# Optimization experiments

Measured on AMD Instinct MI355X. Metric: run time of the kernel, lower is better.

## Reference

```python
import jax, jax.numpy as jnp
import numpy as np

R_MAX = 32
S_MAX = 2
TOKEN_Z = 128
B, N = 1, 1024
NUM_POS = 2 * R_MAX + 2      # 66 bins for residue-index distance
NUM_TOK = 2 * R_MAX + 2      # 66 bins for token-index distance
NUM_CHAIN = 2 * S_MAX + 2    # 6 bins for chain (symmetry) distance
D_IN = NUM_POS + NUM_TOK + 1 + NUM_CHAIN  # 139 = 4*(r_max+1) + 2*(s_max+1) + 1


def setup_inputs() -> dict:
    key = jax.random.key(0)
    ks = jax.random.split(key, 6)
    asym_id = jax.random.randint(ks[0], (B, N), 0, 4)
    residue_index = jax.random.randint(ks[1], (B, N), 0, 512)
    entity_id = jax.random.randint(ks[2], (B, N), 0, 2)
    token_index = jax.random.randint(ks[3], (B, N), 0, 1024)
    sym_id = jax.random.randint(ks[4], (B, N), 0, 4)
    W = jax.random.normal(ks[5], (D_IN, TOKEN_Z), dtype=jnp.float32) / np.sqrt(D_IN).astype(np.float32)
    return {
        'asym_id': asym_id,
        'residue_index': residue_index,
        'entity_id': entity_id,
        'token_index': token_index,
        'sym_id': sym_id,
        'W': W,
    }


def _bin_indices(asym_id, residue_index, token_index, sym_id):
    """Compute the per-pair bin index for each of the three one-hot features."""
    same_chain = asym_id[:, :, None] == asym_id[:, None, :]            # [B,N,N]
    same_residue = residue_index[:, :, None] == residue_index[:, None, :]

    d_res = jnp.clip(residue_index[:, :, None] - residue_index[:, None, :] + R_MAX, 0, 2 * R_MAX)
    d_res = jnp.where(same_chain, d_res, 2 * R_MAX + 1)

    d_tok = jnp.clip(token_index[:, :, None] - token_index[:, None, :] + R_MAX, 0, 2 * R_MAX)
    d_tok = jnp.where(same_chain & same_residue, d_tok, 2 * R_MAX + 1)

    d_chain = jnp.clip(sym_id[:, :, None] - sym_id[:, None, :] + S_MAX, 0, 2 * S_MAX)
    d_chain = jnp.where(same_chain, 2 * S_MAX + 1, d_chain)
    return d_res, d_tok, d_chain


def reference(asym_id, residue_index, entity_id, token_index, sym_id, W):
    # Fused gather-sum: one_hot(d) @ W_block == W_block[d], so the concat of
    # one-hots followed by LinearNoBias equals a sum of 3 row-gathers from W
    # plus the same-entity flag times one W row. Identical math to the
    # original, without materializing the [B,N,N,139] one-hot/concat tensor.
    d_res, d_tok, d_chain = _bin_indices(asym_id, residue_index, token_index, sym_id)
    same_entity = (entity_id[:, :, None] == entity_id[:, None, :]).astype(W.dtype)  # [B,N,N]

    W_pos = W[:NUM_POS]                                  # [66, Z]
    W_tok = W[NUM_POS:NUM_POS + NUM_TOK]                 # [66, Z]
    w_ent = W[NUM_POS + NUM_TOK]                         # [Z]
    W_chain = W[NUM_POS + NUM_TOK + 1:]                  # [6, Z]

    p = W_pos[d_res] + W_tok[d_tok] + W_chain[d_chain] + same_entity[..., None] * w_ent
    return p  # [B, N, N, token_z]
```

## Files before the change

kernel.cpp:

```cpp
#include <hip/hip_runtime.h>


#define N_TOK   1024
#define R_MAX   32
#define S_MAX   2
#define ROW_POS   0
#define ROW_TOK   66
#define ROW_ENT   132
#define ROW_CHAIN 133

__global__ __launch_bounds__(256) void relpos_kernel(
    const int*   __restrict__ asym_id,
    const int*   __restrict__ residue_index,
    const int*   __restrict__ entity_id,
    const int*   __restrict__ token_index,
    const int*   __restrict__ sym_id,
    const float* __restrict__ W,
    float*       __restrict__ out)
{
    __shared__ int s_idx[64];

    const int tid = threadIdx.x;
    const int i   = blockIdx.x >> 4;
    const int j0  = (blockIdx.x & 15) << 6;

    if (tid < 64) {
        const int j  = j0 + tid;
        const int ai = asym_id[i],       aj = asym_id[j];
        const int ri = residue_index[i], rj = residue_index[j];
        const int ti = token_index[i],   tj = token_index[j];
        const int si = sym_id[i],        sj = sym_id[j];
        const int ei = entity_id[i],     ej = entity_id[j];

        const bool same_chain = (ai == aj);
        const bool same_res   = (ri == rj);

        int d_res = min(max(ri - rj + R_MAX, 0), 2 * R_MAX);
        if (!same_chain) d_res = 2 * R_MAX + 1;

        int d_tok = min(max(ti - tj + R_MAX, 0), 2 * R_MAX);
        if (!(same_chain && same_res)) d_tok = 2 * R_MAX + 1;

        const int d_chain = same_chain ? (2 * S_MAX + 1)
                                       : min(max(si - sj + S_MAX, 0), 2 * S_MAX);
        const int ent = (ei == ej) ? 1 : 0;

        s_idx[tid] = d_res | (d_tok << 7) | (d_chain << 14) | (ent << 17);
    }
    __syncthreads();

    const int slot    = tid & 31;
    const int plocal0 = tid >> 5;

    const float4* __restrict__ W4 = (const float4*)W;
    const float4 e = W4[ROW_ENT * 32 + slot];

    float4* __restrict__ outp = (float4*)out + ((long long)blockIdx.x << 11);

    #pragma unroll
    for (int iter = 0; iter < 8; ++iter) {
        const int pl      = plocal0 + iter * 8;
        const int packed  = s_idx[pl];
        const int d_res   =  packed        & 127;
        const int d_tok   = (packed >> 7)  & 127;
        const int d_chain = (packed >> 14) & 7;
        const float m     = (packed & (1 << 17)) ? 1.0f : 0.0f;

        const float4 a = W4[(ROW_POS   + d_res)   * 32 + slot];
        const float4 b = W4[(ROW_TOK   + d_tok)   * 32 + slot];
        const float4 c = W4[(ROW_CHAIN + d_chain) * 32 + slot];

        float4 r;
        r.x = a.x + b.x + c.x + m * e.x;
        r.y = a.y + b.y + c.y + m * e.y;
        r.z = a.z + b.z + c.z + m * e.z;
        r.w = a.w + b.w + c.w + m * e.w;

        outp[pl * 32 + slot] = r;
    }
}

extern "C" void kernel_launch(void* const* d_in, const int* in_sizes, int n_in,
                              void* d_out, int out_size, void* d_ws, size_t ws_size,
                              hipStream_t stream) {
    const int*   asym_id       = (const int*)d_in[0];
    const int*   residue_index = (const int*)d_in[1];
    const int*   entity_id     = (const int*)d_in[2];
    const int*   token_index   = (const int*)d_in[3];
    const int*   sym_id        = (const int*)d_in[4];
    const float* W             = (const float*)d_in[5];
    float*       out           = (float*)d_out;

    const int grid  = (N_TOK * N_TOK) / 64;
    const int block = 256;

    relpos_kernel<<<grid, block, 0, stream>>>(
        asym_id, residue_index, entity_id, token_index, sym_id, W, out);
}
```

Before: 106.4 us.

## Precompute combined row table so each pair output is a single gather

Adds a small pre-kernel that precomputes all 270 reachable sums of position, token, chain and entity rows into a workspace table. The main kernel then computes one combined index per pair and copies one table row, replacing three gathers plus adds. This cuts L2/L1 gather traffic and ALU work per output element, at the cost of an extra kernel launch. It needs enough workspace and falls back to the original direct kernel otherwise.

```diff
diff --git a/kernel.cpp b/kernel.cpp
--- a/kernel.cpp
+++ b/kernel.cpp
@@ -8,17 +8,57 @@
 #define ROW_TOK   66
 #define ROW_ENT   132
 #define ROW_CHAIN 133
+#define TBL_BASE  135
+#define TBL_ROWS  270
+#define TBL_BYTES (TBL_ROWS * 128 * 4)
 
-__global__ __launch_bounds__(256) void relpos_kernel(
+__global__ __launch_bounds__(256) void build_table(
+    const float* __restrict__ W, float* __restrict__ tbl)
+{
+    const int t = blockIdx.x * blockDim.x + threadIdx.x;
+    if (t >= TBL_ROWS * 32) return;
+    const int id   = t >> 5;
+    const int slot = t & 31;
+    const int ent  = (id >= TBL_BASE) ? 1 : 0;
+    const int base = id - ent * TBL_BASE;
+
+    const float4* __restrict__ W4 = (const float4*)W;
+    float4 p, k, c;
+    if (base < 5) {
+        p = W4[(ROW_POS   + 65)   * 32 + slot];
+        k = W4[(ROW_TOK   + 65)   * 32 + slot];
+        c = W4[(ROW_CHAIN + base) * 32 + slot];
+    } else if (base < 70) {
+        p = W4[(ROW_POS + (base - 5)) * 32 + slot];
+        k = W4[(ROW_TOK   + 65)   * 32 + slot];
+        c = W4[(ROW_CHAIN + 5)    * 32 + slot];
+    } else {
+        p = W4[(ROW_POS   + 32)   * 32 + slot];
+        k = W4[(ROW_TOK + (base - 70)) * 32 + slot];
+        c = W4[(ROW_CHAIN + 5)    * 32 + slot];
+    }
+    float4 r;
+    r.x = p.x + k.x + c.x;
+    r.y = p.y + k.y + c.y;
+    r.z = p.z + k.z + c.z;
+    r.w = p.w + k.w + c.w;
+    if (ent) {
+        const float4 e = W4[ROW_ENT * 32 + slot];
+        r.x += e.x; r.y += e.y; r.z += e.z; r.w += e.w;
+    }
+    ((float4*)tbl)[id * 32 + slot] = r;
+}
+
+__global__ __launch_bounds__(256) void relpos_tbl(
     const int*   __restrict__ asym_id,
     const int*   __restrict__ residue_index,
     const int*   __restrict__ entity_id,
     const int*   __restrict__ token_index,
     const int*   __restrict__ sym_id,
-    const float* __restrict__ W,
+    const float* __restrict__ tbl,
     float*       __restrict__ out)
 {
-    __shared__ int s_idx[64];
+    __shared__ int s_id[64];
 
     const int tid = threadIdx.x;
     const int i   = blockIdx.x >> 4;
@@ -32,29 +72,70 @@
         const int si = sym_id[i],        sj = sym_id[j];
         const int ei = entity_id[i],     ej = entity_id[j];
 
+        int base;
+        if (ai != aj) {
+            base = min(max(si - sj + S_MAX, 0), 2 * S_MAX);
+        } else if (ri != rj) {
+            base = 5 + min(max(ri - rj + R_MAX, 0), 2 * R_MAX);
+        } else {
+            base = 70 + min(max(ti - tj + R_MAX, 0), 2 * R_MAX);
+        }
+        s_id[tid] = base + ((ei == ej) ? TBL_BASE : 0);
+    }
+    __syncthreads();
+
+    const int slot    = tid & 31;
+    const int plocal0 = tid >> 5;
+
+    const float4* __restrict__ T4 = (const float4*)tbl;
+    float4* __restrict__ outp = (float4*)out + ((long long)blockIdx.x << 11);
+
+    #pragma unroll
+    for (int iter = 0; iter < 8; ++iter) {
+        const int pl = plocal0 + iter * 8;
+        const int id = s_id[pl];
+        outp[pl * 32 + slot] = T4[id * 32 + slot];
+    }
+}
+
+__global__ __launch_bounds__(256) void relpos_direct(
+    const int*   __restrict__ asym_id,
+    const int*   __restrict__ residue_index,
+    const int*   __restrict__ entity_id,
+    const int*   __restrict__ token_index,
+    const int*   __restrict__ sym_id,
+    const float* __restrict__ W,
+    float*       __restrict__ out)
+{
+    __shared__ int s_idx[64];
+    const int tid = threadIdx.x;
+    const int i   = blockIdx.x >> 4;
+    const int j0  = (blockIdx.x & 15) << 6;
+
+    if (tid < 64) {
+        const int j  = j0 + tid;
+        const int ai = asym_id[i],       aj = asym_id[j];
+        const int ri = residue_index[i], rj = residue_index[j];
+        const int ti = token_index[i],   tj = token_index[j];
+        const int si = sym_id[i],        sj = sym_id[j];
+        const int ei = entity_id[i],     ej = entity_id[j];
         const bool same_chain = (ai == aj);
         const bool same_res   = (ri == rj);
-
         int d_res = min(max(ri - rj + R_MAX, 0), 2 * R_MAX);
         if (!same_chain) d_res = 2 * R_MAX + 1;
-
         int d_tok = min(max(ti - tj + R_MAX, 0), 2 * R_MAX);
         if (!(same_chain && same_res)) d_tok = 2 * R_MAX + 1;
-
         const int d_chain = same_chain ? (2 * S_MAX + 1)
                                        : min(max(si - sj + S_MAX, 0), 2 * S_MAX);
         const int ent = (ei == ej) ? 1 : 0;
-
         s_idx[tid] = d_res | (d_tok << 7) | (d_chain << 14) | (ent << 17);
     }
     __syncthreads();
 
     const int slot    = tid & 31;
     const int plocal0 = tid >> 5;
-
     const float4* __restrict__ W4 = (const float4*)W;
     const float4 e = W4[ROW_ENT * 32 + slot];
-
     float4* __restrict__ outp = (float4*)out + ((long long)blockIdx.x << 11);
 
     #pragma unroll
@@ -65,17 +146,14 @@
         const int d_tok   = (packed >> 7)  & 127;
         const int d_chain = (packed >> 14) & 7;
         const float m     = (packed & (1 << 17)) ? 1.0f : 0.0f;
-
         const float4 a = W4[(ROW_POS   + d_res)   * 32 + slot];
         const float4 b = W4[(ROW_TOK   + d_tok)   * 32 + slot];
         const float4 c = W4[(ROW_CHAIN + d_chain) * 32 + slot];
-
         float4 r;
         r.x = a.x + b.x + c.x + m * e.x;
         r.y = a.y + b.y + c.y + m * e.y;
         r.z = a.z + b.z + c.z + m * e.z;
         r.w = a.w + b.w + c.w + m * e.w;
-
         outp[pl * 32 + slot] = r;
     }
 }
@@ -94,6 +172,13 @@
     const int grid  = (N_TOK * N_TOK) / 64;
     const int block = 256;
 
-    relpos_kernel<<<grid, block, 0, stream>>>(
-        asym_id, residue_index, entity_id, token_index, sym_id, W, out);
+    if (ws_size >= (size_t)TBL_BYTES) {
+        float* tbl = (float*)d_ws;
+        build_table<<<(TBL_ROWS * 32 + 255) / 256, 256, 0, stream>>>(W, tbl);
+        relpos_tbl<<<grid, block, 0, stream>>>(
+            asym_id, residue_index, entity_id, token_index, sym_id, tbl, out);
+    } else {
+        relpos_direct<<<grid, block, 0, stream>>>(
+            asym_id, residue_index, entity_id, token_index, sym_id, W, out);
+    }
 }
```

Result: slower. 110.1 us (+3.5%).

## Process eight tiles per block with double-buffered index computation

Applied to the files above, without the earlier changes.

Each block now handles eight 64-pair tiles instead of one, so the grid shrinks eightfold. While the current tile is gathered and written, the first wave precomputes the packed bin indices for the next tile into a second shared buffer. The aim is to cut block launch overhead and hide the index-load latency. The cost is a __syncthreads per tile and fewer blocks to spread across the GPU.

```diff
diff --git a/kernel.cpp b/kernel.cpp
--- a/kernel.cpp
+++ b/kernel.cpp
@@ -9,6 +9,36 @@
 #define ROW_ENT   132
 #define ROW_CHAIN 133
 
+#define TILES_PER_BLOCK 8
+#define NUM_BLOCKS ((N_TOK * N_TOK / 64) / TILES_PER_BLOCK)
+
+__device__ __forceinline__ int pack_idx(
+    const int* __restrict__ asym_id, const int* __restrict__ residue_index,
+    const int* __restrict__ entity_id, const int* __restrict__ token_index,
+    const int* __restrict__ sym_id, int i, int j)
+{
+    const int ai = asym_id[i],       aj = asym_id[j];
+    const int ri = residue_index[i], rj = residue_index[j];
+    const int ti = token_index[i],   tj = token_index[j];
+    const int si = sym_id[i],        sj = sym_id[j];
+    const int ei = entity_id[i],     ej = entity_id[j];
+
+    const bool same_chain = (ai == aj);
+    const bool same_res   = (ri == rj);
+
+    int d_res = min(max(ri - rj + R_MAX, 0), 2 * R_MAX);
+    if (!same_chain) d_res = 2 * R_MAX + 1;
+
+    int d_tok = min(max(ti - tj + R_MAX, 0), 2 * R_MAX);
+    if (!(same_chain && same_res)) d_tok = 2 * R_MAX + 1;
+
+    const int d_chain = same_chain ? (2 * S_MAX + 1)
+                                   : min(max(si - sj + S_MAX, 0), 2 * S_MAX);
+    const int ent = (ei == ej) ? 1 : 0;
+
+    return d_res | (d_tok << 7) | (d_chain << 14) | (ent << 17);
+}
+
 __global__ __launch_bounds__(256) void relpos_kernel(
     const int*   __restrict__ asym_id,
     const int*   __restrict__ residue_index,
@@ -18,34 +48,17 @@
     const float* __restrict__ W,
     float*       __restrict__ out)
 {
-    __shared__ int s_idx[64];
+    __shared__ int s_id[2][64];
 
-    const int tid = threadIdx.x;
-    const int i   = blockIdx.x >> 4;
-    const int j0  = (blockIdx.x & 15) << 6;
+    const int tid   = threadIdx.x;
+    const int tile0 = blockIdx.x * TILES_PER_BLOCK;
 
     if (tid < 64) {
-        const int j  = j0 + tid;
-        const int ai = asym_id[i],       aj = asym_id[j];
-        const int ri = residue_index[i], rj = residue_index[j];
-        const int ti = token_index[i],   tj = token_index[j];
-        const int si = sym_id[i],        sj = sym_id[j];
-        const int ei = entity_id[i],     ej = entity_id[j];
-
-        const bool same_chain = (ai == aj);
-        const bool same_res   = (ri == rj);
-
-        int d_res = min(max(ri - rj + R_MAX, 0), 2 * R_MAX);
-        if (!same_chain) d_res = 2 * R_MAX + 1;
-
-        int d_tok = min(max(ti - tj + R_MAX, 0), 2 * R_MAX);
-        if (!(same_chain && same_res)) d_tok = 2 * R_MAX + 1;
-
-        const int d_chain = same_chain ? (2 * S_MAX + 1)
-                                       : min(max(si - sj + S_MAX, 0), 2 * S_MAX);
-        const int ent = (ei == ej) ? 1 : 0;
-
-        s_idx[tid] = d_res | (d_tok << 7) | (d_chain << 14) | (ent << 17);
+        const int tile = tile0;
+        const int i  = tile >> 4;
+        const int j  = ((tile & 15) << 6) + tid;
+        s_id[0][tid] = pack_idx(asym_id, residue_index, entity_id,
+                                token_index, sym_id, i, j);
     }
     __syncthreads();
 
@@ -55,28 +68,43 @@
     const float4* __restrict__ W4 = (const float4*)W;
     const float4 e = W4[ROW_ENT * 32 + slot];
 
-    float4* __restrict__ outp = (float4*)out + ((long long)blockIdx.x << 11);
+    for (int t = 0; t < TILES_PER_BLOCK; ++t) {
+        const int buf = t & 1;
 
-    #pragma unroll
-    for (int iter = 0; iter < 8; ++iter) {
-        const int pl      = plocal0 + iter * 8;
-        const int packed  = s_idx[pl];
-        const int d_res   =  packed        & 127;
-        const int d_tok   = (packed >> 7)  & 127;
-        const int d_chain = (packed >> 14) & 7;
-        const float m     = (packed & (1 << 17)) ? 1.0f : 0.0f;
+        if (t + 1 < TILES_PER_BLOCK && tid < 64) {
+            const int tile = tile0 + t + 1;
+            const int i  = tile >> 4;
+            const int j  = ((tile & 15) << 6) + tid;
+            s_id[buf ^ 1][tid] = pack_idx(asym_id, residue_index, entity_id,
+                                          token_index, sym_id, i, j);
+        }
 
-        const float4 a = W4[(ROW_POS   + d_res)   * 32 + slot];
-        const float4 b = W4[(ROW_TOK   + d_tok)   * 32 + slot];
-        const float4 c = W4[(ROW_CHAIN + d_chain) * 32 + slot];
+        float4* __restrict__ outp =
+            (float4*)out + ((long long)(tile0 + t) << 11);
 
-        float4 r;
-        r.x = a.x + b.x + c.x + m * e.x;
-        r.y = a.y + b.y + c.y + m * e.y;
-        r.z = a.z + b.z + c.z + m * e.z;
-        r.w = a.w + b.w + c.w + m * e.w;
+        #pragma unroll
+        for (int iter = 0; iter < 8; ++iter) {
+            const int pl      = plocal0 + iter * 8;
+            const int packed  = s_id[buf][pl];
+            const int d_res   =  packed        & 127;
+            const int d_tok   = (packed >> 7)  & 127;
+            const int d_chain = (packed >> 14) & 7;
+            const float m     = (packed & (1 << 17)) ? 1.0f : 0.0f;
 
-        outp[pl * 32 + slot] = r;
+            const float4 a = W4[(ROW_POS   + d_res)   * 32 + slot];
+            const float4 b = W4[(ROW_TOK   + d_tok)   * 32 + slot];
+            const float4 c = W4[(ROW_CHAIN + d_chain) * 32 + slot];
+
+            float4 r;
+            r.x = a.x + b.x + c.x + m * e.x;
+            r.y = a.y + b.y + c.y + m * e.y;
+            r.z = a.z + b.z + c.z + m * e.z;
+            r.w = a.w + b.w + c.w + m * e.w;
+
+            outp[pl * 32 + slot] = r;
+        }
+
+        __syncthreads();
     }
 }
 
@@ -91,9 +119,6 @@
     const float* W             = (const float*)d_in[5];
     float*       out           = (float*)d_out;
 
-    const int grid  = (N_TOK * N_TOK) / 64;
-    const int block = 256;
-
-    relpos_kernel<<<grid, block, 0, stream>>>(
+    relpos_kernel<<<NUM_BLOCKS, 256, 0, stream>>>(
         asym_id, residue_index, entity_id, token_index, sym_id, W, out);
 }
```

After: 105.4 us. No clear change (-1.0%).
